# Kernel tuning notes

Hardware: AMD Instinct MI355X
Metric: run time of the kernel (lower is better)

Reference implementation:

```python
import jax, jax.numpy as jnp
import numpy as np

N_NODES = 100000
N_EDGES = 1600000
IN_DIM, HID_DIM, OUT_DIM = 128, 128, 64


def setup_inputs() -> dict:
    key = jax.random.key(0)
    k1, k2, k3, k4 = jax.random.split(key, 4)
    x = jax.random.normal(k1, (N_NODES, IN_DIM), dtype=jnp.float32)
    edge_index = jax.random.randint(k2, (2, N_EDGES), 0, N_NODES, dtype=jnp.int32)
    # Glorot-ish init for weights
    W1 = jax.random.normal(k3, (IN_DIM, HID_DIM), dtype=jnp.float32) / np.sqrt(IN_DIM)
    W2 = jax.random.normal(k4, (HID_DIM, OUT_DIM), dtype=jnp.float32) / np.sqrt(HID_DIM)
    b1 = jnp.zeros((HID_DIM,), dtype=jnp.float32)
    b2 = jnp.zeros((OUT_DIM,), dtype=jnp.float32)
    return {"x": x, "edge_index": edge_index, "W1": W1, "b1": b1, "W2": W2, "b2": b2}


def _gcn_norm(edge_index, num_nodes):
    # PyG gcn_norm: add self-loops, symmetric normalization deg^-1/2 A deg^-1/2
    loops = jnp.arange(num_nodes, dtype=edge_index.dtype)
    src = jnp.concatenate([edge_index[0], loops])  # [E+N]
    tgt = jnp.concatenate([edge_index[1], loops])
    deg = jax.ops.segment_sum(jnp.ones_like(tgt, dtype=jnp.float32), tgt,
                              num_segments=num_nodes)
    dinv = jnp.where(deg > 0, jax.lax.rsqrt(deg), 0.0)
    norm = dinv[src] * dinv[tgt]  # [E+N]
    return src, tgt, norm


def _gcn_conv(x, W, b, src, tgt, norm, num_nodes):
    h = x @ W                              # [N, D_out] transform first (GCNConv order)
    msg = norm[:, None] * h[src]           # gather + scale per edge
    agg = jax.ops.segment_sum(msg, tgt, num_segments=num_nodes)  # scatter-add
    return agg + b


def reference(x, edge_index, W1, b1, W2, b2):
    n = x.shape[0]
    src, tgt, norm = _gcn_norm(edge_index, n)
    h = jax.nn.relu(_gcn_conv(x, W1, b1, src, tgt, norm, n))
    out = _gcn_conv(h, W2, b2, src, tgt, norm, n)
    return out
```

## Files before the change

### kernel.cpp

```cpp
#include <hip/hip_runtime.h>


typedef unsigned int uint;
typedef unsigned short ushort;
typedef __attribute__((ext_vector_type(8))) short bf16x8;
typedef __attribute__((ext_vector_type(8))) ushort u16x8;
typedef __attribute__((ext_vector_type(4))) float f32x4;

#define BSHIFT 8
#define MAXBK  512
#define NB     256
#define CAP    8192

__device__ inline ushort f2bf(float f) {
    uint u = __float_as_uint(f);
    return (ushort)((u + 0x7fffu + ((u >> 16) & 1u)) >> 16);
}
__device__ inline float bf_lo(uint u) { return __uint_as_float(u << 16); }
__device__ inline float bf_hi(uint u) { return __uint_as_float(u & 0xffff0000u); }

__global__ __launch_bounds__(256) void hist_kernel(const int* __restrict__ tgt,
                                                   int* __restrict__ counts,
                                                   int E, int chunk, int nbk) {
    __shared__ int hist[MAXBK];
    int t = threadIdx.x, b = blockIdx.x;
    for (int i = t; i < nbk; i += 256) hist[i] = 0;
    __syncthreads();
    int s = b * chunk, e = min(E, s + chunk);
    int i = s + t * 4;
    for (; i + 3 < e; i += 1024) {
        int4 tv = *(const int4*)&tgt[i];
        atomicAdd(&hist[tv.x >> BSHIFT], 1);
        atomicAdd(&hist[tv.y >> BSHIFT], 1);
        atomicAdd(&hist[tv.z >> BSHIFT], 1);
        atomicAdd(&hist[tv.w >> BSHIFT], 1);
    }
    if (i < e)
        for (int k = i; k < e; ++k) atomicAdd(&hist[tgt[k] >> BSHIFT], 1);
    __syncthreads();
    for (int i2 = t; i2 < nbk; i2 += 256) counts[i2 * NB + b] = hist[i2];
}

__global__ __launch_bounds__(256) void scan_partial(const int* __restrict__ in,
                                                    int* __restrict__ bsum, int M) {
    int t = threadIdx.x, b = blockIdx.x;
    int base = b * 1024 + t * 4;
    int s = 0;
#pragma unroll
    for (int k = 0; k < 4; ++k) s += (base + k < M) ? in[base + k] : 0;
#pragma unroll
    for (int off = 32; off > 0; off >>= 1) s += __shfl_down(s, off, 64);
    __shared__ int ws[4];
    if ((t & 63) == 0) ws[t >> 6] = s;
    __syncthreads();
    if (t == 0) bsum[b] = ws[0] + ws[1] + ws[2] + ws[3];
}

__global__ __launch_bounds__(256) void scan_final_counts(int* __restrict__ counts,
                                                         const int* __restrict__ bsum,
                                                         int M) {
    int t = threadIdx.x, b = blockIdx.x;
    int lane = t & 63, wid = t >> 6;
    int p = 0;
    for (int i = t; i < b; i += 256) p += bsum[i];
#pragma unroll
    for (int off = 32; off > 0; off >>= 1) p += __shfl_down(p, off, 64);
    __shared__ int ps[4];
    if (lane == 0) ps[wid] = p;
    __syncthreads();
    int pre = ps[0] + ps[1] + ps[2] + ps[3];

    int base = b * 1024 + t * 4;
    int d[4];
#pragma unroll
    for (int k = 0; k < 4; ++k) d[k] = (base + k < M) ? counts[base + k] : 0;
    int tot = d[0] + d[1] + d[2] + d[3];
    int incl = tot;
#pragma unroll
    for (int off = 1; off < 64; off <<= 1) {
        int u = __shfl_up(incl, off, 64);
        if (lane >= off) incl += u;
    }
    __shared__ int wsum[4];
    if (lane == 63) wsum[wid] = incl;
    __syncthreads();
    int woff = 0;
    for (int w = 0; w < wid; ++w) woff += wsum[w];
    int run = incl - tot + woff + pre;
#pragma unroll
    for (int k = 0; k < 4; ++k) {
        if (base + k < M) counts[base + k] = run;
        run += d[k];
    }
}

__global__ __launch_bounds__(256) void bucket_scatter(const int* __restrict__ src,
                                                      const int* __restrict__ tgt,
                                                      const int* __restrict__ offsets,
                                                      int* __restrict__ tmpP,
                                                      int E, int chunk, int nbk) {
    __shared__ int cur[MAXBK];
    int t = threadIdx.x, b = blockIdx.x;
    for (int i = t; i < nbk; i += 256) cur[i] = offsets[i * NB + b];
    __syncthreads();
    int s = b * chunk, e = min(E, s + chunk);
    int i = s + t * 4;
    for (; i + 3 < e; i += 1024) {
        int4 sv = *(const int4*)&src[i];
        int4 tv = *(const int4*)&tgt[i];
        int p0 = atomicAdd(&cur[tv.x >> BSHIFT], 1);
        tmpP[p0] = (sv.x << BSHIFT) | (tv.x & 255);
        int p1 = atomicAdd(&cur[tv.y >> BSHIFT], 1);
        tmpP[p1] = (sv.y << BSHIFT) | (tv.y & 255);
        int p2 = atomicAdd(&cur[tv.z >> BSHIFT], 1);
        tmpP[p2] = (sv.z << BSHIFT) | (tv.z & 255);
        int p3 = atomicAdd(&cur[tv.w >> BSHIFT], 1);
        tmpP[p3] = (sv.w << BSHIFT) | (tv.w & 255);
    }
    if (i < e) {
        for (int k = i; k < e; ++k) {
            int tg = tgt[k];
            int p = atomicAdd(&cur[tg >> BSHIFT], 1);
            tmpP[p] = (src[k] << BSHIFT) | (tg & 255);
        }
    }
}

__global__ __launch_bounds__(256) void bucket_finish(const int* __restrict__ tmpP,
                                                     const int* __restrict__ offsets,
                                                     int* __restrict__ rowptr,
                                                     float* __restrict__ dinv,
                                                     int* __restrict__ csr_src,
                                                     int N, int E, int nbk) {
    __shared__ int stage[CAP];
    __shared__ int cnt[256];
    __shared__ int wsum[4];
    int t = threadIdx.x, b = blockIdx.x;
    cnt[t] = 0;
    __syncthreads();
    int s = offsets[b * NB];
    int e = (b + 1 < nbk) ? offsets[(b + 1) * NB] : E;
    int m = e - s;
    for (int i = t; i < m; i += 256) {
        int ed = tmpP[s + i];
        if (i < CAP) stage[i] = ed;
        atomicAdd(&cnt[ed & 255], 1);
    }
    __syncthreads();
    int lane = t & 63, wid = t >> 6;
    int d = cnt[t];
    int incl = d;
#pragma unroll
    for (int off = 1; off < 64; off <<= 1) {
        int u = __shfl_up(incl, off, 64);
        if (lane >= off) incl += u;
    }
    if (lane == 63) wsum[wid] = incl;
    __syncthreads();
    int woff = 0;
    for (int w = 0; w < wid; ++w) woff += wsum[w];
    int excl = s + incl - d + woff;
    int node = b * 256 + t;
    if (node < N) {
        rowptr[node] = excl;
        dinv[node] = rsqrtf((float)d + 1.0f);
    }
    if (b == nbk - 1 && t == 255) rowptr[N] = E;
    cnt[t] = excl;
    __syncthreads();
    for (int i = t; i < m; i += 256) {
        int ed = (i < CAP) ? stage[i] : tmpP[s + i];
        int p = atomicAdd(&cnt[ed & 255], 1);
        csr_src[p] = ed >> BSHIFT;
    }
}

template <int M, typename AT>
__device__ inline void gemm_impl(const AT* __restrict__ A,
                                 const float* __restrict__ W,
                                 const float* __restrict__ dinv,
                                 ushort* __restrict__ C, int N) {
    constexpr int WTS = 136;
    __shared__ ushort WT[M * WTS];
    const int tid = threadIdx.x;
    for (int i = tid; i < 128 * (M / 4); i += 256) {
        int k = i / (M / 4);
        int n0 = (i % (M / 4)) * 4;
        float4 w = *(const float4*)&W[k * M + n0];
        WT[(n0 + 0) * WTS + k] = f2bf(w.x);
        WT[(n0 + 1) * WTS + k] = f2bf(w.y);
        WT[(n0 + 2) * WTS + k] = f2bf(w.z);
        WT[(n0 + 3) * WTS + k] = f2bf(w.w);
    }
    __syncthreads();

    const int wv = tid >> 6, lane = tid & 63;
    const int quad = lane >> 4, mrow = lane & 15;
    const int r0 = blockIdx.x * 128 + wv * 16 + mrow;
    const int r1 = r0 + 64;
    const int a0i = min(r0, N - 1);
    const int a1i = min(r1, N - 1);

    f32x4 acc0[M / 16], acc1[M / 16];
#pragma unroll
    for (int t = 0; t < M / 16; ++t) {
        acc0[t] = (f32x4){0.f, 0.f, 0.f, 0.f};
        acc1[t] = (f32x4){0.f, 0.f, 0.f, 0.f};
    }

#pragma unroll
    for (int ks = 0; ks < 4; ++ks) {
        const int k0 = ks * 32 + quad * 8;
        bf16x8 af0, af1;
        if constexpr (sizeof(AT) == 4) {
            const float* ar0 = (const float*)A + (size_t)a0i * 128;
            const float* ar1 = (const float*)A + (size_t)a1i * 128;
            float4 x0 = *(const float4*)&ar0[k0];
            float4 y0 = *(const float4*)&ar0[k0 + 4];
            float4 x1 = *(const float4*)&ar1[k0];
            float4 y1 = *(const float4*)&ar1[k0 + 4];
            af0[0] = (short)f2bf(x0.x); af0[1] = (short)f2bf(x0.y);
            af0[2] = (short)f2bf(x0.z); af0[3] = (short)f2bf(x0.w);
            af0[4] = (short)f2bf(y0.x); af0[5] = (short)f2bf(y0.y);
            af0[6] = (short)f2bf(y0.z); af0[7] = (short)f2bf(y0.w);
            af1[0] = (short)f2bf(x1.x); af1[1] = (short)f2bf(x1.y);
            af1[2] = (short)f2bf(x1.z); af1[3] = (short)f2bf(x1.w);
            af1[4] = (short)f2bf(y1.x); af1[5] = (short)f2bf(y1.y);
            af1[6] = (short)f2bf(y1.z); af1[7] = (short)f2bf(y1.w);
        } else {
            af0 = *(const bf16x8*)((const ushort*)A + (size_t)a0i * 128 + k0);
            af1 = *(const bf16x8*)((const ushort*)A + (size_t)a1i * 128 + k0);
        }
#pragma unroll
        for (int t = 0; t < M / 16; ++t) {
            bf16x8 bfr = *(const bf16x8*)&WT[(t * 16 + mrow) * WTS + k0];
            acc0[t] = __builtin_amdgcn_mfma_f32_16x16x32_bf16(af0, bfr, acc0[t], 0, 0, 0);
            acc1[t] = __builtin_amdgcn_mfma_f32_16x16x32_bf16(af1, bfr, acc1[t], 0, 0, 0);
        }
    }

    const int ob0 = blockIdx.x * 128 + wv * 16 + quad * 4;
#pragma unroll
    for (int r = 0; r < 4; ++r) {
        int o0 = ob0 + r;
        if (o0 < N) {
            float dv = dinv[o0];
#pragma unroll
            for (int t = 0; t < M / 16; ++t)
                C[(size_t)o0 * M + t * 16 + mrow] = f2bf(dv * acc0[t][r]);
        }
        int o1 = ob0 + 64 + r;
        if (o1 < N) {
            float dv = dinv[o1];
#pragma unroll
            for (int t = 0; t < M / 16; ++t)
                C[(size_t)o1 * M + t * 16 + mrow] = f2bf(dv * acc1[t][r]);
        }
    }
}

__global__ __launch_bounds__(256) void gemm1_k(const float* __restrict__ A,
                                               const float* __restrict__ W,
                                               const float* __restrict__ dinv,
                                               ushort* __restrict__ C, int N) {
    gemm_impl<128, float>(A, W, dinv, C, N);
}
__global__ __launch_bounds__(256) void gemm2_k(const ushort* __restrict__ A,
                                               const float* __restrict__ W,
                                               const float* __restrict__ dinv,
                                               ushort* __restrict__ C, int N) {
    gemm_impl<64, ushort>(A, W, dinv, C, N);
}

template <int D, bool RELU, bool OUTBF>
__device__ inline void gather_impl(
    const ushort* __restrict__ h, const int* __restrict__ rowptr,
    const int* __restrict__ csr_src, const float* __restrict__ dinv,
    const float* __restrict__ bias, void* __restrict__ outv,
    int nodeBeg, int nodeLim) {
    constexpr int Q = D / 8;
    constexpr int G = 64 / Q;
    const int wid = threadIdx.x >> 6, lane = threadIdx.x & 63;
    const int node = nodeBeg + blockIdx.x * 4 + wid;
    if (node >= nodeLim) return;
    const int g = lane / Q, q = lane % Q;
    const int qoff = q * 8;
    const int beg = rowptr[node], end = rowptr[node + 1];
    float acc[8] = {};

    auto acc8 = [&](uint4 v) {
        acc[0] += bf_lo(v.x); acc[1] += bf_hi(v.x);
        acc[2] += bf_lo(v.y); acc[3] += bf_hi(v.y);
        acc[4] += bf_lo(v.z); acc[5] += bf_hi(v.z);
        acc[6] += bf_lo(v.w); acc[7] += bf_hi(v.w);
    };
    auto acc8m = [&](uint4 v, float m) {
        acc[0] += m * bf_lo(v.x); acc[1] += m * bf_hi(v.x);
        acc[2] += m * bf_lo(v.y); acc[3] += m * bf_hi(v.y);
        acc[4] += m * bf_lo(v.z); acc[5] += m * bf_hi(v.z);
        acc[6] += m * bf_lo(v.w); acc[7] += m * bf_hi(v.w);
    };

    int j = beg;
    for (; j + 4 * G <= end; j += 4 * G) {
        int s0 = csr_src[j + g];
        int s1 = csr_src[j + G + g];
        int s2 = csr_src[j + 2 * G + g];
        int s3 = csr_src[j + 3 * G + g];
        uint4 v0 = *(const uint4*)&h[(size_t)s0 * D + qoff];
        uint4 v1 = *(const uint4*)&h[(size_t)s1 * D + qoff];
        uint4 v2 = *(const uint4*)&h[(size_t)s2 * D + qoff];
        uint4 v3 = *(const uint4*)&h[(size_t)s3 * D + qoff];
        acc8(v0); acc8(v1); acc8(v2); acc8(v3);
    }
    for (; j < end; j += 2 * G) {
        int e0 = j + g, e1 = j + G + g;
        bool b0 = e0 < end, b1 = e1 < end;
        int s0 = b0 ? csr_src[e0] : 0;
        int s1 = b1 ? csr_src[e1] : 0;
        float m0 = b0 ? 1.0f : 0.0f;
        float m1 = b1 ? 1.0f : 0.0f;
        uint4 va = *(const uint4*)&h[(size_t)s0 * D + qoff];
        uint4 vb = *(const uint4*)&h[(size_t)s1 * D + qoff];
        acc8m(va, m0); acc8m(vb, m1);
    }
#pragma unroll
    for (int m2 = Q; m2 < 64; m2 <<= 1)
#pragma unroll
        for (int k = 0; k < 8; ++k) acc[k] += __shfl_xor(acc[k], m2, 64);

    {
        uint4 hv = *(const uint4*)&h[(size_t)node * D + qoff];
        acc8(hv);
    }
    if (g == 0) {
        const float di = dinv[node];
        float4 b0 = *(const float4*)&bias[qoff];
        float4 b1 = *(const float4*)&bias[qoff + 4];
        float r[8] = {di * acc[0] + b0.x, di * acc[1] + b0.y,
                      di * acc[2] + b0.z, di * acc[3] + b0.w,
                      di * acc[4] + b1.x, di * acc[5] + b1.y,
                      di * acc[6] + b1.z, di * acc[7] + b1.w};
        if (RELU) {
#pragma unroll
            for (int k = 0; k < 8; ++k) r[k] = fmaxf(r[k], 0.0f);
        }
        if constexpr (OUTBF) {
            ushort* out = (ushort*)outv;
            u16x8 o;
#pragma unroll
            for (int k = 0; k < 8; ++k) o[k] = f2bf(r[k]);
            *(u16x8*)&out[(size_t)node * D + qoff] = o;
        } else {
            float* out = (float*)outv;
            *(float4*)&out[(size_t)node * D + qoff]     = make_float4(r[0], r[1], r[2], r[3]);
            *(float4*)&out[(size_t)node * D + qoff + 4] = make_float4(r[4], r[5], r[6], r[7]);
        }
    }
}

__global__ __launch_bounds__(256) void gather1_k(
    const ushort* __restrict__ h, const int* __restrict__ rowptr,
    const int* __restrict__ csr_src, const float* __restrict__ dinv,
    const float* __restrict__ bias, void* __restrict__ outv,
    int nodeBeg, int nodeLim) {
    gather_impl<128, true, true>(h, rowptr, csr_src, dinv, bias, outv,
                                 nodeBeg, nodeLim);
}
__global__ __launch_bounds__(256) void gather2_k(
    const ushort* __restrict__ h, const int* __restrict__ rowptr,
    const int* __restrict__ csr_src, const float* __restrict__ dinv,
    const float* __restrict__ bias, void* __restrict__ outv,
    int nodeBeg, int nodeLim) {
    gather_impl<64, false, false>(h, rowptr, csr_src, dinv, bias, outv,
                                  nodeBeg, nodeLim);
}

extern "C" void kernel_launch(void* const* d_in, const int* in_sizes, int n_in,
                              void* d_out, int out_size, void* d_ws, size_t ws_size,
                              hipStream_t stream) {
    const float* x  = (const float*)d_in[0];
    const int*   ei = (const int*)d_in[1];
    const float* W1 = (const float*)d_in[2];
    const float* b1 = (const float*)d_in[3];
    const float* W2 = (const float*)d_in[4];
    const float* b2 = (const float*)d_in[5];
    float* out = (float*)d_out;

    const int N = in_sizes[0] / 128;
    const int E = in_sizes[1] / 2;
    const int* src = ei;
    const int* tgt = ei + E;

    const int nbk   = (N + 255) >> BSHIFT;
    const int chunk = (((E + NB - 1) / NB) + 3) & ~3;
    const int Mc    = nbk * NB;

    float* ws = (float*)d_ws;
    const size_t Np = (size_t)((N + 3) & ~3);
    float*  dinv    = ws;
    int*    rowptr  = (int*)(ws + Np);
    int*    counts  = rowptr + Np + 4;
    int*    bsum    = counts + MAXBK * NB;
    int*    csr_src = bsum + 128;
    int*    tmpP    = csr_src + E;
    ushort* h       = (ushort*)(tmpP + E);
    ushort* h1      = h + (size_t)N * 128;
    ushort* h2      = h;

    const int nbc = (Mc + 1023) / 1024;

    hist_kernel<<<NB, 256, 0, stream>>>(tgt, counts, E, chunk, nbk);
    scan_partial<<<nbc, 256, 0, stream>>>(counts, bsum, Mc);
    scan_final_counts<<<nbc, 256, 0, stream>>>(counts, bsum, Mc);
    bucket_scatter<<<NB, 256, 0, stream>>>(src, tgt, counts, tmpP, E, chunk, nbk);
    bucket_finish<<<nbk, 256, 0, stream>>>(tmpP, counts, rowptr, dinv, csr_src, N, E, nbk);

    gemm1_k<<<(N + 127) / 128, 256, 0, stream>>>(x, W1, dinv, h, N);
    {
        const int Nq = (N + 3) / 4;
        for (int qd = 0; qd < 4; ++qd) {
            int nb = qd * Nq, nl = min(N, nb + Nq);
            if (nb >= nl) break;
            gather1_k<<<((nl - nb) + 3) / 4, 256, 0, stream>>>(
                h, rowptr, csr_src, dinv, b1, h1, nb, nl);
        }
    }

    gemm2_k<<<(N + 127) / 128, 256, 0, stream>>>(h1, W2, dinv, h2, N);
    gather2_k<<<(N + 3) / 4, 256, 0, stream>>>(
        h2, rowptr, csr_src, dinv, b2, out, 0, N);
}
```

Measured before the change: 331.0 us.

## Fuse second-layer GEMM into first gather epilogue and split gather2 launch

The layer-1 aggregation kernel now applies bias and ReLU, stages the 128-wide row in shared memory, and multiplies it by W2 (converted to bf16 in LDS per block) to write the dinv-scaled 64-wide h2 directly. This removes the separate gemm2 kernel and the write and re-read of the h1 intermediate. In exchange, every gather block reloads and converts all of W2 into 16KB of LDS, the per-node matmul runs on scalar FMAs instead of MFMA, and blocks do an early return before the __syncthreads-free LDS use. The second gather is also split into two launches over node halves.

```diff
diff --git a/kernel.cpp b/kernel.cpp
--- a/kernel.cpp
+++ b/kernel.cpp
@@ -18,6 +18,7 @@
 }
 __device__ inline float bf_lo(uint u) { return __uint_as_float(u << 16); }
 __device__ inline float bf_hi(uint u) { return __uint_as_float(u & 0xffff0000u); }
+__device__ inline float bf2f(ushort u) { return __uint_as_float((uint)u << 16); }
 
 __global__ __launch_bounds__(256) void hist_kernel(const int* __restrict__ tgt,
                                                    int* __restrict__ counts,
@@ -175,11 +176,11 @@
     }
 }
 
-template <int M, typename AT>
-__device__ inline void gemm_impl(const AT* __restrict__ A,
-                                 const float* __restrict__ W,
-                                 const float* __restrict__ dinv,
-                                 ushort* __restrict__ C, int N) {
+__global__ __launch_bounds__(256) void gemm1_k(const float* __restrict__ A,
+                                               const float* __restrict__ W,
+                                               const float* __restrict__ dinv,
+                                               ushort* __restrict__ C, int N) {
+    constexpr int M = 128;
     constexpr int WTS = 136;
     __shared__ ushort WT[M * WTS];
     const int tid = threadIdx.x;
@@ -212,25 +213,20 @@
     for (int ks = 0; ks < 4; ++ks) {
         const int k0 = ks * 32 + quad * 8;
         bf16x8 af0, af1;
-        if constexpr (sizeof(AT) == 4) {
-            const float* ar0 = (const float*)A + (size_t)a0i * 128;
-            const float* ar1 = (const float*)A + (size_t)a1i * 128;
-            float4 x0 = *(const float4*)&ar0[k0];
-            float4 y0 = *(const float4*)&ar0[k0 + 4];
-            float4 x1 = *(const float4*)&ar1[k0];
-            float4 y1 = *(const float4*)&ar1[k0 + 4];
-            af0[0] = (short)f2bf(x0.x); af0[1] = (short)f2bf(x0.y);
-            af0[2] = (short)f2bf(x0.z); af0[3] = (short)f2bf(x0.w);
-            af0[4] = (short)f2bf(y0.x); af0[5] = (short)f2bf(y0.y);
-            af0[6] = (short)f2bf(y0.z); af0[7] = (short)f2bf(y0.w);
-            af1[0] = (short)f2bf(x1.x); af1[1] = (short)f2bf(x1.y);
-            af1[2] = (short)f2bf(x1.z); af1[3] = (short)f2bf(x1.w);
-            af1[4] = (short)f2bf(y1.x); af1[5] = (short)f2bf(y1.y);
-            af1[6] = (short)f2bf(y1.z); af1[7] = (short)f2bf(y1.w);
-        } else {
-            af0 = *(const bf16x8*)((const ushort*)A + (size_t)a0i * 128 + k0);
-            af1 = *(const bf16x8*)((const ushort*)A + (size_t)a1i * 128 + k0);
-        }
+        const float* ar0 = A + (size_t)a0i * 128;
+        const float* ar1 = A + (size_t)a1i * 128;
+        float4 x0 = *(const float4*)&ar0[k0];
+        float4 y0 = *(const float4*)&ar0[k0 + 4];
+        float4 x1 = *(const float4*)&ar1[k0];
+        float4 y1 = *(const float4*)&ar1[k0 + 4];
+        af0[0] = (short)f2bf(x0.x); af0[1] = (short)f2bf(x0.y);
+        af0[2] = (short)f2bf(x0.z); af0[3] = (short)f2bf(x0.w);
+        af0[4] = (short)f2bf(y0.x); af0[5] = (short)f2bf(y0.y);
+        af0[6] = (short)f2bf(y0.z); af0[7] = (short)f2bf(y0.w);
+        af1[0] = (short)f2bf(x1.x); af1[1] = (short)f2bf(x1.y);
+        af1[2] = (short)f2bf(x1.z); af1[3] = (short)f2bf(x1.w);
+        af1[4] = (short)f2bf(y1.x); af1[5] = (short)f2bf(y1.y);
+        af1[6] = (short)f2bf(y1.z); af1[7] = (short)f2bf(y1.w);
 #pragma unroll
         for (int t = 0; t < M / 16; ++t) {
             bf16x8 bfr = *(const bf16x8*)&WT[(t * 16 + mrow) * WTS + k0];
@@ -259,31 +255,26 @@
     }
 }
 
-__global__ __launch_bounds__(256) void gemm1_k(const float* __restrict__ A,
-                                               const float* __restrict__ W,
-                                               const float* __restrict__ dinv,
-                                               ushort* __restrict__ C, int N) {
-    gemm_impl<128, float>(A, W, dinv, C, N);
-}
-__global__ __launch_bounds__(256) void gemm2_k(const ushort* __restrict__ A,
-                                               const float* __restrict__ W,
-                                               const float* __restrict__ dinv,
-                                               ushort* __restrict__ C, int N) {
-    gemm_impl<64, ushort>(A, W, dinv, C, N);
-}
-
-template <int D, bool RELU, bool OUTBF>
-__device__ inline void gather_impl(
+__global__ __launch_bounds__(256) void gather1f_k(
     const ushort* __restrict__ h, const int* __restrict__ rowptr,
     const int* __restrict__ csr_src, const float* __restrict__ dinv,
-    const float* __restrict__ bias, void* __restrict__ outv,
-    int nodeBeg, int nodeLim) {
-    constexpr int Q = D / 8;
-    constexpr int G = 64 / Q;
-    const int wid = threadIdx.x >> 6, lane = threadIdx.x & 63;
+    const float* __restrict__ bias, const float* __restrict__ W2,
+    ushort* __restrict__ h2, int nodeBeg, int nodeLim) {
+    constexpr int D = 128;
+    constexpr int Q = 16, G = 4;
+    __shared__ ushort W2L[16 * 64 * 8];
+    __shared__ ushort rowL[4 * 128];
+    const int tid = threadIdx.x;
+    for (int i = tid; i < 8192; i += 256) {
+        int k = i >> 6, j = i & 63;
+        W2L[(k >> 3) * 512 + j * 8 + (k & 7)] = f2bf(W2[k * 64 + j]);
+    }
+    __syncthreads();
+
+    const int wid = tid >> 6, lane = tid & 63;
     const int node = nodeBeg + blockIdx.x * 4 + wid;
     if (node >= nodeLim) return;
-    const int g = lane / Q, q = lane % Q;
+    const int g = lane >> 4, q = lane & 15;
     const int qoff = q * 8;
     const int beg = rowptr[node], end = rowptr[node + 1];
     float acc[8] = {};
@@ -333,47 +324,101 @@
         uint4 hv = *(const uint4*)&h[(size_t)node * D + qoff];
         acc8(hv);
     }
+    const float di = dinv[node];
     if (g == 0) {
-        const float di = dinv[node];
         float4 b0 = *(const float4*)&bias[qoff];
         float4 b1 = *(const float4*)&bias[qoff + 4];
         float r[8] = {di * acc[0] + b0.x, di * acc[1] + b0.y,
                       di * acc[2] + b0.z, di * acc[3] + b0.w,
                       di * acc[4] + b1.x, di * acc[5] + b1.y,
                       di * acc[6] + b1.z, di * acc[7] + b1.w};
-        if (RELU) {
-#pragma unroll
-            for (int k = 0; k < 8; ++k) r[k] = fmaxf(r[k], 0.0f);
-        }
-        if constexpr (OUTBF) {
-            ushort* out = (ushort*)outv;
-            u16x8 o;
-#pragma unroll
-            for (int k = 0; k < 8; ++k) o[k] = f2bf(r[k]);
-            *(u16x8*)&out[(size_t)node * D + qoff] = o;
-        } else {
-            float* out = (float*)outv;
-            *(float4*)&out[(size_t)node * D + qoff]     = make_float4(r[0], r[1], r[2], r[3]);
-            *(float4*)&out[(size_t)node * D + qoff + 4] = make_float4(r[4], r[5], r[6], r[7]);
-        }
-    }
-}
-
-__global__ __launch_bounds__(256) void gather1_k(
-    const ushort* __restrict__ h, const int* __restrict__ rowptr,
-    const int* __restrict__ csr_src, const float* __restrict__ dinv,
-    const float* __restrict__ bias, void* __restrict__ outv,
-    int nodeBeg, int nodeLim) {
-    gather_impl<128, true, true>(h, rowptr, csr_src, dinv, bias, outv,
-                                 nodeBeg, nodeLim);
-}
+        u16x8 o;
+#pragma unroll
+        for (int k = 0; k < 8; ++k) o[k] = f2bf(fmaxf(r[k], 0.0f));
+        *(u16x8*)&rowL[wid * 128 + qoff] = o;
+    }
+    float acc2 = 0.0f;
+#pragma unroll
+    for (int c = 0; c < 16; ++c) {
+        u16x8 rv = *(const u16x8*)&rowL[wid * 128 + c * 8];
+        u16x8 wv = *(const u16x8*)&W2L[c * 512 + lane * 8];
+#pragma unroll
+        for (int e = 0; e < 8; ++e) acc2 += bf2f(rv[e]) * bf2f(wv[e]);
+    }
+    h2[(size_t)node * 64 + lane] = f2bf(di * acc2);
+}
+
 __global__ __launch_bounds__(256) void gather2_k(
     const ushort* __restrict__ h, const int* __restrict__ rowptr,
     const int* __restrict__ csr_src, const float* __restrict__ dinv,
-    const float* __restrict__ bias, void* __restrict__ outv,
+    const float* __restrict__ bias, float* __restrict__ out,
     int nodeBeg, int nodeLim) {
-    gather_impl<64, false, false>(h, rowptr, csr_src, dinv, bias, outv,
-                                  nodeBeg, nodeLim);
+    constexpr int D = 64;
+    constexpr int Q = 8, G = 8;
+    const int wid = threadIdx.x >> 6, lane = threadIdx.x & 63;
+    const int node = nodeBeg + blockIdx.x * 4 + wid;
+    if (node >= nodeLim) return;
+    const int g = lane / Q, q = lane % Q;
+    const int qoff = q * 8;
+    const int beg = rowptr[node], end = rowptr[node + 1];
+    float acc[8] = {};
+
+    auto acc8 = [&](uint4 v) {
+        acc[0] += bf_lo(v.x); acc[1] += bf_hi(v.x);
+        acc[2] += bf_lo(v.y); acc[3] += bf_hi(v.y);
+        acc[4] += bf_lo(v.z); acc[5] += bf_hi(v.z);
+        acc[6] += bf_lo(v.w); acc[7] += bf_hi(v.w);
+    };
+    auto acc8m = [&](uint4 v, float m) {
+        acc[0] += m * bf_lo(v.x); acc[1] += m * bf_hi(v.x);
+        acc[2] += m * bf_lo(v.y); acc[3] += m * bf_hi(v.y);
+        acc[4] += m * bf_lo(v.z); acc[5] += m * bf_hi(v.z);
+        acc[6] += m * bf_lo(v.w); acc[7] += m * bf_hi(v.w);
+    };
+
+    int j = beg;
+    for (; j + 4 * G <= end; j += 4 * G) {
+        int s0 = csr_src[j + g];
+        int s1 = csr_src[j + G + g];
+        int s2 = csr_src[j + 2 * G + g];
+        int s3 = csr_src[j + 3 * G + g];
+        uint4 v0 = *(const uint4*)&h[(size_t)s0 * D + qoff];
+        uint4 v1 = *(const uint4*)&h[(size_t)s1 * D + qoff];
+        uint4 v2 = *(const uint4*)&h[(size_t)s2 * D + qoff];
+        uint4 v3 = *(const uint4*)&h[(size_t)s3 * D + qoff];
+        acc8(v0); acc8(v1); acc8(v2); acc8(v3);
+    }
+    for (; j < end; j += 2 * G) {
+        int e0 = j + g, e1 = j + G + g;
+        bool b0 = e0 < end, b1 = e1 < end;
+        int s0 = b0 ? csr_src[e0] : 0;
+        int s1 = b1 ? csr_src[e1] : 0;
+        float m0 = b0 ? 1.0f : 0.0f;
+        float m1 = b1 ? 1.0f : 0.0f;
+        uint4 va = *(const uint4*)&h[(size_t)s0 * D + qoff];
+        uint4 vb = *(const uint4*)&h[(size_t)s1 * D + qoff];
+        acc8m(va, m0); acc8m(vb, m1);
+    }
+#pragma unroll
+    for (int m2 = Q; m2 < 64; m2 <<= 1)
+#pragma unroll
+        for (int k = 0; k < 8; ++k) acc[k] += __shfl_xor(acc[k], m2, 64);
+
+    {
+        uint4 hv = *(const uint4*)&h[(size_t)node * D + qoff];
+        acc8(hv);
+    }
+    if (g == 0) {
+        const float di = dinv[node];
+        float4 b0 = *(const float4*)&bias[qoff];
+        float4 b1 = *(const float4*)&bias[qoff + 4];
+        *(float4*)&out[(size_t)node * D + qoff] =
+            make_float4(di * acc[0] + b0.x, di * acc[1] + b0.y,
+                        di * acc[2] + b0.z, di * acc[3] + b0.w);
+        *(float4*)&out[(size_t)node * D + qoff + 4] =
+            make_float4(di * acc[4] + b1.x, di * acc[5] + b1.y,
+                        di * acc[6] + b1.z, di * acc[7] + b1.w);
+    }
 }
 
 extern "C" void kernel_launch(void* const* d_in, const int* in_sizes, int n_in,
@@ -405,8 +450,7 @@
     int*    csr_src = bsum + 128;
     int*    tmpP    = csr_src + E;
     ushort* h       = (ushort*)(tmpP + E);
-    ushort* h1      = h + (size_t)N * 128;
-    ushort* h2      = h;
+    ushort* h2      = h + (size_t)N * 128;
 
     const int nbc = (Mc + 1023) / 1024;
 
@@ -417,17 +461,24 @@
     bucket_finish<<<nbk, 256, 0, stream>>>(tmpP, counts, rowptr, dinv, csr_src, N, E, nbk);
 
     gemm1_k<<<(N + 127) / 128, 256, 0, stream>>>(x, W1, dinv, h, N);
+
     {
         const int Nq = (N + 3) / 4;
         for (int qd = 0; qd < 4; ++qd) {
             int nb = qd * Nq, nl = min(N, nb + Nq);
             if (nb >= nl) break;
-            gather1_k<<<((nl - nb) + 3) / 4, 256, 0, stream>>>(
-                h, rowptr, csr_src, dinv, b1, h1, nb, nl);
-        }
-    }
-
-    gemm2_k<<<(N + 127) / 128, 256, 0, stream>>>(h1, W2, dinv, h2, N);
-    gather2_k<<<(N + 3) / 4, 256, 0, stream>>>(
-        h2, rowptr, csr_src, dinv, b2, out, 0, N);
-}
+            gather1f_k<<<((nl - nb) + 3) / 4, 256, 0, stream>>>(
+                h, rowptr, csr_src, dinv, b1, W2, h2, nb, nl);
+        }
+    }
+
+    {
+        const int Nh = (N + 1) / 2;
+        for (int hd = 0; hd < 2; ++hd) {
+            int nb = hd * Nh, nl = min(N, nb + Nh);
+            if (nb >= nl) break;
+            gather2_k<<<((nl - nb) + 3) / 4, 256, 0, stream>>>(
+                h2, rowptr, csr_src, dinv, b2, out, nb, nl);
+        }
+    }
+}
```

Measured after the change: 372.1 us. 12.4% more time.
